# Performance work log

Measured on AMD Instinct MI355X. Metric: run time of the kernel, lower is better.

Reference implementation:

```python
import jax, jax.numpy as jnp
import numpy as np

N_NODES = 100000
N_EDGES = 1000000
EDGE_F = 64
IN_C = 128
OUT_C = 256


def setup_inputs() -> dict:
    key = jax.random.key(0)
    k1, k2, k3, k4, k5, k6, k7 = jax.random.split(key, 7)
    edge_index = jax.random.randint(k1, (2, N_EDGES), 0, N_NODES, dtype=jnp.int64 if jax.config.read('jax_enable_x64') else jnp.int32)
    edge_attr = jax.random.normal(k2, (N_EDGES, EDGE_F), dtype=jnp.float32)
    node_attr = jax.random.normal(k3, (N_NODES, IN_C), dtype=jnp.float32)
    edge_weight = jax.random.uniform(k4, (N_EDGES,), dtype=jnp.float32)
    node_weight = jax.random.uniform(k5, (N_NODES,), dtype=jnp.float32)
    W = jax.random.normal(k6, (IN_C + EDGE_F, OUT_C), dtype=jnp.float32) * (1.0 / np.sqrt(IN_C + EDGE_F))
    b = jax.random.normal(k7, (OUT_C,), dtype=jnp.float32) * 0.01
    return {"edge_index": edge_index, "edge_attr": edge_attr, "node_attr": node_attr,
            "edge_weight": edge_weight, "node_weight": node_weight, "W": W, "b": b}


def reference(edge_index, edge_attr, node_attr, edge_weight, node_weight, W, b):
    num_nodes = node_attr.shape[0]
    # per-edge weighting
    ea = edge_attr * edge_weight[:, None]                       # [E, F]
    tgt = edge_index[0]                                         # [E]
    # scatter_mean over target nodes
    sums = jax.ops.segment_sum(ea, tgt, num_segments=num_nodes)                 # [N, F]
    cnt = jax.ops.segment_sum(jnp.ones_like(edge_weight), tgt, num_segments=num_nodes)  # [N]
    mean = sums / jnp.maximum(cnt, 1.0)[:, None]                # zeros for empty segments
    mean = mean * node_weight[:, None]
    x = jnp.concatenate([node_attr, mean], axis=1)              # [N, C+F]
    return jax.nn.relu(x @ W + b)                               # [N, OUT_C]
```

## Files before the change

kernel.cpp:

```cpp
#include <hip/hip_runtime.h>
#include <hip/hip_bf16.h>

#define NN 100000
#define NE 1000000
#define EF 64
#define IC 128
#define OC 256
#define CAP 48

typedef __attribute__((ext_vector_type(8))) short bf16x8;
typedef __attribute__((ext_vector_type(4))) float f32x4;

static __device__ __forceinline__ ushort f2bf(float f) {
  unsigned u = __float_as_uint(f);
  u += 0x7fffu + ((u >> 16) & 1u);
  return (ushort)(u >> 16);
}

__global__ __launch_bounds__(256) void wprep_kernel(
    const float* __restrict__ W, ushort* __restrict__ wfrag,
    int* __restrict__ cnt) {
  int t = blockIdx.x * 256 + threadIdx.x;
  int i = t & 7;
  int lane = (t >> 3) & 63;
  int ct = (t >> 9) & 15;
  int s = t >> 13;
  int k = s * 32 + (lane >> 4) * 8 + i;
  int col = ct * 16 + (lane & 15);
  wfrag[t] = f2bf(W[(size_t)k * OC + col]);
  for (int j = t; j < NN; j += 192 * 256) cnt[j] = 0;
}

__global__ __launch_bounds__(256) void place_kernel(const int4* __restrict__ tgt4,
                                                    const float4* __restrict__ ew4,
                                                    int* __restrict__ cnt,
                                                    int2* __restrict__ epack) {
  int q = blockIdx.x * 256 + threadIdx.x;
  if (q < NE / 4) {
    int4 t = tgt4[q];
    float4 w = ew4[q];
    int e = q * 4;
    int p;
    p = atomicAdd(&cnt[t.x], 1);
    if (p < CAP) epack[(size_t)t.x * CAP + p] = make_int2(e,     __float_as_int(w.x));
    p = atomicAdd(&cnt[t.y], 1);
    if (p < CAP) epack[(size_t)t.y * CAP + p] = make_int2(e + 1, __float_as_int(w.y));
    p = atomicAdd(&cnt[t.z], 1);
    if (p < CAP) epack[(size_t)t.z * CAP + p] = make_int2(e + 2, __float_as_int(w.z));
    p = atomicAdd(&cnt[t.w], 1);
    if (p < CAP) epack[(size_t)t.w * CAP + p] = make_int2(e + 3, __float_as_int(w.w));
  }
}

__global__ __launch_bounds__(256) void agg_kernel(
    const int* __restrict__ cnt, const int2* __restrict__ epack,
    const float* __restrict__ ea, const float* __restrict__ nwt,
    ushort* __restrict__ mean_bf) {
  int lane = threadIdx.x & 63;
  int n = blockIdx.x * 4 + (threadIdx.x >> 6);
  if (n >= NN) return;
  int deg = cnt[n];
  const int2* strip = epack + (size_t)n * CAP;
  int eg = lane >> 4;
  int fq = lane & 15;

  f32x4 acc = (f32x4)(0.0f);
  for (int j = 0; j < deg; j += 16) {
#pragma unroll
    for (int u = 0; u < 4; ++u) {
      int i = j + u * 4 + eg;
      int c = min(i, deg - 1);
      int2 m = strip[c];
      float w = (i < deg) ? __int_as_float(m.y) : 0.0f;
      f32x4 v = *(const f32x4*)(ea + (size_t)m.x * EF + fq * 4);
      acc += v * w;
    }
  }

#pragma unroll
  for (int m = 16; m <= 32; m <<= 1) {
    f32x4 o;
#pragma unroll
    for (int i = 0; i < 4; ++i) o[i] = __shfl_xor(acc[i], m, 64);
    acc += o;
  }

  if (lane < 16) {
    float scale = nwt[n] / (float)max(deg, 1);
    ushort4 o;
    o.x = f2bf(acc[0] * scale);
    o.y = f2bf(acc[1] * scale);
    o.z = f2bf(acc[2] * scale);
    o.w = f2bf(acc[3] * scale);
    *(ushort4*)(mean_bf + (size_t)n * EF + fq * 4) = o;
  }
}

__global__ __launch_bounds__(256) void gemm_kernel(
    const float* __restrict__ na, const ushort* __restrict__ mean_bf,
    const ushort* __restrict__ wfrag, const float* __restrict__ bias,
    float* __restrict__ out) {
  int tid = threadIdx.x;
  int lane = tid & 63;
  int wv = tid >> 6;
  int row_base = blockIdx.x * 64 + wv * 16;
  int r = row_base + (lane & 15);
  int rc = min(r, NN - 1);
  int kofs = (lane >> 4) * 8;
  int colb = lane & 15;

  const float* narow = na + (size_t)rc * IC;
  const ushort* mrow = mean_bf + (size_t)rc * EF;

  bf16x8 afrag[6];
#pragma unroll
  for (int s = 0; s < 4; ++s) {
    f32x4 lo = *(const f32x4*)(narow + s * 32 + kofs);
    f32x4 hi = *(const f32x4*)(narow + s * 32 + kofs + 4);
#pragma unroll
    for (int i = 0; i < 4; ++i) {
      afrag[s][i] = (short)f2bf(lo[i]);
      afrag[s][4 + i] = (short)f2bf(hi[i]);
    }
  }
#pragma unroll
  for (int s = 0; s < 2; ++s)
    afrag[4 + s] = *(const bf16x8*)(mrow + s * 32 + kofs);

  f32x4 acc[16];
#pragma unroll
  for (int ct = 0; ct < 16; ++ct) acc[ct] = (f32x4)(0.0f);

#pragma unroll
  for (int s = 0; s < 6; ++s) {
#pragma unroll
    for (int ct = 0; ct < 16; ++ct) {
      bf16x8 bfrag =
          *(const bf16x8*)(wfrag + ((size_t)((s * 16 + ct) * 64 + lane) * 8));
      acc[ct] =
          __builtin_amdgcn_mfma_f32_16x16x32_bf16(afrag[s], bfrag, acc[ct], 0, 0, 0);
    }
  }

#pragma unroll
  for (int ct = 0; ct < 16; ++ct) {
    int col = ct * 16 + colb;
    float bv = bias[col];
#pragma unroll
    for (int i = 0; i < 4; ++i) {
      int rr = row_base + (lane >> 4) * 4 + i;
      if (rr < NN) {
        float v = fmaxf(acc[ct][i] + bv, 0.0f);
        __builtin_nontemporal_store(v, out + (size_t)rr * OC + col);
      }
    }
  }
}

extern "C" void kernel_launch(void* const* d_in, const int* in_sizes, int n_in,
                              void* d_out, int out_size, void* d_ws, size_t ws_size,
                              hipStream_t stream) {
  const int* edge_index = (const int*)d_in[0];
  const float* edge_attr = (const float*)d_in[1];
  const float* node_attr = (const float*)d_in[2];
  const float* edge_weight = (const float*)d_in[3];
  const float* node_weight = (const float*)d_in[4];
  const float* W = (const float*)d_in[5];
  const float* bias = (const float*)d_in[6];
  float* out = (float*)d_out;

  char* p = (char*)d_ws;
  ushort* mean_bf = (ushort*)p;
  int2* epack    = (int2*)(p + 12800000);
  int* cnt       = (int*)(p + 51200000);
  ushort* wfrag  = (ushort*)(p + 51600000);

  wprep_kernel<<<192, 256, 0, stream>>>(W, wfrag, cnt);
  place_kernel<<<(NE / 4 + 255) / 256, 256, 0, stream>>>(
      (const int4*)edge_index, (const float4*)edge_weight, cnt, epack);
  agg_kernel<<<(NN + 3) / 4, 256, 0, stream>>>(cnt, epack, edge_attr,
                                               node_weight, mean_bf);
  gemm_kernel<<<(NN + 63) / 64, 256, 0, stream>>>(node_attr, mean_bf, wfrag,
                                                  bias, out);
}
```

Before: 234.5 us.

## Map four nodes per wavefront in aggregation, dropping cross-lane reduction

The aggregation kernel now assigns each 16-lane quarter of a wavefront to its own node, rather than spreading one node's edges across the four quarters. Each quarter walks its node's edge list serially in chunks of 8, so the shuffle reduction and the idle-lane store are gone and the block count falls by four. The loop bound is the maximum degree among the four nodes, so lanes with shorter lists run masked iterations. Degree imbalance within a wavefront can therefore waste loads.

Measured after the change: 229.5 us. 2.1% less time.

```diff
diff --git a/kernel.cpp b/kernel.cpp
--- a/kernel.cpp
+++ b/kernel.cpp
@@ -57,43 +57,40 @@
     const float* __restrict__ ea, const float* __restrict__ nwt,
     ushort* __restrict__ mean_bf) {
   int lane = threadIdx.x & 63;
-  int n = blockIdx.x * 4 + (threadIdx.x >> 6);
-  if (n >= NN) return;
+  int wv = threadIdx.x >> 6;
+  int ns = lane >> 4;
+  int fq = lane & 15;
+  int n = blockIdx.x * 16 + wv * 4 + ns;
+
   int deg = cnt[n];
+  int dclamp = max(deg - 1, 0);
   const int2* strip = epack + (size_t)n * CAP;
-  int eg = lane >> 4;
-  int fq = lane & 15;
+
+  int md = deg;
+  md = max(md, __shfl_xor(md, 16, 64));
+  md = max(md, __shfl_xor(md, 32, 64));
 
   f32x4 acc = (f32x4)(0.0f);
-  for (int j = 0; j < deg; j += 16) {
+  for (int j = 0; j < md; j += 8) {
 #pragma unroll
-    for (int u = 0; u < 4; ++u) {
-      int i = j + u * 4 + eg;
-      int c = min(i, deg - 1);
+    for (int u = 0; u < 8; ++u) {
+      int jj = j + u;
+      int c = min(jj, dclamp);
       int2 m = strip[c];
-      float w = (i < deg) ? __int_as_float(m.y) : 0.0f;
-      f32x4 v = *(const f32x4*)(ea + (size_t)m.x * EF + fq * 4);
+      float w = (jj < deg) ? __int_as_float(m.y) : 0.0f;
+      int e = (deg > 0) ? m.x : 0;
+      f32x4 v = *(const f32x4*)(ea + (size_t)e * EF + fq * 4);
       acc += v * w;
     }
   }
 
-#pragma unroll
-  for (int m = 16; m <= 32; m <<= 1) {
-    f32x4 o;
-#pragma unroll
-    for (int i = 0; i < 4; ++i) o[i] = __shfl_xor(acc[i], m, 64);
-    acc += o;
-  }
-
-  if (lane < 16) {
-    float scale = nwt[n] / (float)max(deg, 1);
-    ushort4 o;
-    o.x = f2bf(acc[0] * scale);
-    o.y = f2bf(acc[1] * scale);
-    o.z = f2bf(acc[2] * scale);
-    o.w = f2bf(acc[3] * scale);
-    *(ushort4*)(mean_bf + (size_t)n * EF + fq * 4) = o;
-  }
+  float scale = nwt[n] / (float)max(deg, 1);
+  ushort4 o;
+  o.x = f2bf(acc[0] * scale);
+  o.y = f2bf(acc[1] * scale);
+  o.z = f2bf(acc[2] * scale);
+  o.w = f2bf(acc[3] * scale);
+  *(ushort4*)(mean_bf + (size_t)n * EF + fq * 4) = o;
 }
 
 __global__ __launch_bounds__(256) void gemm_kernel(
@@ -178,8 +175,8 @@
   wprep_kernel<<<192, 256, 0, stream>>>(W, wfrag, cnt);
   place_kernel<<<(NE / 4 + 255) / 256, 256, 0, stream>>>(
       (const int4*)edge_index, (const float4*)edge_weight, cnt, epack);
-  agg_kernel<<<(NN + 3) / 4, 256, 0, stream>>>(cnt, epack, edge_attr,
-                                               node_weight, mean_bf);
+  agg_kernel<<<NN / 16, 256, 0, stream>>>(cnt, epack, edge_attr,
+                                          node_weight, mean_bf);
   gemm_kernel<<<(NN + 63) / 64, 256, 0, stream>>>(node_attr, mean_bf, wfrag,
                                                   bias, out);
 }
```
